# Kernel tuning notes

Hardware: AMD Instinct MI355X
Metric: run time of the kernel (lower is better)

The kernel has to match this reference:

```python
import jax, jax.numpy as jnp
import numpy as np


def setup_inputs() -> dict:
    key = jax.random.key(0)
    k1, k2 = jax.random.split(key)
    B, N, M = 4, 16384, 4096
    src_points = jax.random.normal(k1, (B, N, 3), dtype=jnp.float32)
    target_verts = jax.random.normal(k2, (B, M, 3), dtype=jnp.float32)
    return {"src_points": src_points, "target_verts": target_verts}


def reference(src_points, target_verts):
    # target_faces=None path of ChamferLoss: degenerate one-vertex triangles,
    # so closest-point-on-mesh == nearest target vertex.
    # d2[b,n,m] = ||p_bn - v_bm||^2 via the expansion p2 + v2 - 2 p.v
    p2 = jnp.sum(src_points * src_points, axis=-1)          # (B, N)
    v2 = jnp.sum(target_verts * target_verts, axis=-1)      # (B, M)
    pv = jnp.einsum('bnd,bmd->bnm', src_points, target_verts)  # (B, N, M)
    d2 = p2[:, :, None] + v2[:, None, :] - 2.0 * pv
    d2 = jnp.maximum(d2, 0.0)
    min_d2 = jnp.min(d2, axis=-1)                            # (B, N)
    num_src_per_batch = src_points.shape[1]
    loss = jnp.sum(min_d2, axis=-1) / num_src_per_batch      # (B,)
    return loss
```

## Files before the change

kernel.cpp:

```cpp
#include <hip/hip_runtime.h>
#include <float.h>


typedef __bf16 bf16x8 __attribute__((ext_vector_type(8)));
typedef float  f32x16 __attribute__((ext_vector_type(16)));

constexpr int B = 4, N = 16384, M = 4096;
constexpr int BN = B * N;
constexpr int TILES = M / 32;
constexpr int HT = TILES / 2;
constexpr int TPB = 512;
constexpr int PPB = 256;
constexpr int NPB = BN / PPB;

constexpr size_t VFRAG_BYTES = (size_t)B * M * 32;

__global__ __launch_bounds__(256) void chamfer_pre(
    const float* __restrict__ tv, unsigned char* __restrict__ vfr,
    float* __restrict__ out)
{
    if (blockIdx.x == 0 && threadIdx.x < B) out[threadIdx.x] = 0.0f;
    int i = blockIdx.x * 256 + threadIdx.x;
    float x = tv[3 * i + 0], y = tv[3 * i + 1], z = tv[3 * i + 2];
    __bf16 xh = (__bf16)x, yh = (__bf16)y, zh = (__bf16)z;
    float xhf = (float)xh, yhf = (float)yh, zhf = (float)zh;
    __bf16 xl = (__bf16)(x - xhf), yl = (__bf16)(y - yhf), zl = (__bf16)(z - zhf);
    float v2 = fmaf(x, x, fmaf(y, y, z * z));
    __bf16 v2h = (__bf16)v2;
    __bf16 v2l = (__bf16)(v2 - (float)v2h);
    __bf16 zero = (__bf16)0.0f;

    bf16x8 h0, h1;
    h0[0] = (__bf16)(-2.0f * xhf); h0[1] = (__bf16)(-2.0f * yhf);
    h0[2] = (__bf16)(-2.0f * zhf);
    h0[3] = h0[0]; h0[4] = h0[1]; h0[5] = h0[2];
    h0[6] = (__bf16)(-2.0f * (float)xl); h0[7] = (__bf16)(-2.0f * (float)yl);
    h1[0] = (__bf16)(-2.0f * (float)zl); h1[1] = v2h; h1[2] = v2l;
    h1[3] = zero; h1[4] = zero; h1[5] = zero; h1[6] = zero; h1[7] = zero;

    int m = i & (M - 1);
    size_t base = (size_t)(i >> 12) * 131072 + (size_t)(m >> 5) * 1024
                + (size_t)(m & 31) * 16;
    *(bf16x8*)(vfr + base)       = h0;
    *(bf16x8*)(vfr + base + 512) = h1;
}

__global__ __launch_bounds__(TPB) void chamfer_main(
    const float* __restrict__ src, const unsigned char* __restrict__ vfr,
    float* __restrict__ out)
{
    const int pblk = blockIdx.x;
    const int b    = pblk >> 6;
    const int t    = threadIdx.x;
    const int w    = t >> 6, L = t & 63;
    const int s    = w & 3, h = w >> 2;
    const int half = L >> 5, c = L & 31;
    const int laneoff = half * 512 + c * 16;

    const int P0 = pblk * PPB + s * 64;
    const int p0 = P0 + c, p1 = P0 + 32 + c;
    float x0 = src[3 * p0], y0 = src[3 * p0 + 1], z0 = src[3 * p0 + 2];
    float x1 = src[3 * p1], y1 = src[3 * p1 + 1], z1 = src[3 * p1 + 2];
    float pp0 = fmaf(x0, x0, fmaf(y0, y0, z0 * z0));
    float pp1 = fmaf(x1, x1, fmaf(y1, y1, z1 * z1));

    __bf16 one = (__bf16)1.0f, zero = (__bf16)0.0f;
    bf16x8 bP0, bP1;
    {
        __bf16 xh = (__bf16)x0, yh = (__bf16)y0, zh = (__bf16)z0;
        __bf16 xl = (__bf16)(x0 - (float)xh), yl = (__bf16)(y0 - (float)yh),
               zl = (__bf16)(z0 - (float)zh);
        if (half == 0) { bP0[0]=xh; bP0[1]=yh; bP0[2]=zh; bP0[3]=xl; bP0[4]=yl; bP0[5]=zl; bP0[6]=xh; bP0[7]=yh; }
        else { bP0[0]=zh; bP0[1]=one; bP0[2]=one; bP0[3]=zero; bP0[4]=zero; bP0[5]=zero; bP0[6]=zero; bP0[7]=zero; }
    }
    {
        __bf16 xh = (__bf16)x1, yh = (__bf16)y1, zh = (__bf16)z1;
        __bf16 xl = (__bf16)(x1 - (float)xh), yl = (__bf16)(y1 - (float)yh),
               zl = (__bf16)(z1 - (float)zh);
        if (half == 0) { bP1[0]=xh; bP1[1]=yh; bP1[2]=zh; bP1[3]=xl; bP1[4]=yl; bP1[5]=zl; bP1[6]=xh; bP1[7]=yh; }
        else { bP1[0]=zh; bP1[1]=one; bP1[2]=one; bP1[3]=zero; bP1[4]=zero; bP1[5]=zero; bP1[6]=zero; bP1[7]=zero; }
    }

    f32x16 zeroC;
#pragma unroll
    for (int r = 0; r < 16; ++r) zeroC[r] = 0.0f;
    float mn0[8], mn1[8];
#pragma unroll
    for (int u = 0; u < 8; ++u) { mn0[u] = FLT_MAX; mn1[u] = FLT_MAX; }

    const unsigned char* abase =
        vfr + (size_t)b * 131072 + (size_t)h * (HT * 1024) + laneoff;
#pragma unroll 8
    for (int tt = 0; tt < HT; ++tt) {
        bf16x8 av = *(const bf16x8*)(abase + tt * 1024);
        f32x16 C0 = __builtin_amdgcn_mfma_f32_32x32x16_bf16(av, bP0, zeroC, 0, 0, 0);
        f32x16 C1 = __builtin_amdgcn_mfma_f32_32x32x16_bf16(av, bP1, zeroC, 0, 0, 0);
#pragma unroll
        for (int u = 0; u < 8; ++u) {
            mn0[u] = fminf(fminf(mn0[u], C0[2 * u]), C0[2 * u + 1]);
            mn1[u] = fminf(fminf(mn1[u], C1[2 * u]), C1[2 * u + 1]);
        }
    }

    float a01 = fminf(fminf(mn0[0], mn0[1]), fminf(mn0[2], mn0[3]));
    float a23 = fminf(fminf(mn0[4], mn0[5]), fminf(mn0[6], mn0[7]));
    float m0 = fminf(a01, a23);
    m0 = fminf(m0, __shfl_xor(m0, 32, 64));
    float b01 = fminf(fminf(mn1[0], mn1[1]), fminf(mn1[2], mn1[3]));
    float b23 = fminf(fminf(mn1[4], mn1[5]), fminf(mn1[6], mn1[7]));
    float m1 = fminf(b01, b23);
    m1 = fminf(m1, __shfl_xor(m1, 32, 64));
    float m  = half ? m1 : m0;
    float pp = half ? pp1 : pp0;

    __shared__ float lds_m[TPB];
    __shared__ float acc[8];
    lds_m[t] = m;
    __syncthreads();

    float sum = 0.0f;
    if (w < 4) {
        float mm = fminf(m, lds_m[t + 256]);
        sum = fmaxf(mm + pp, 0.0f);
    }
    for (int off = 32; off > 0; off >>= 1)
        sum += __shfl_down(sum, off, 64);
    if (L == 0) acc[w] = sum;
    __syncthreads();
    if (t == 0) {
        float ssum = acc[0] + acc[1] + acc[2] + acc[3];
        atomicAdd(&out[b], ssum * (1.0f / N));
    }
}

extern "C" void kernel_launch(void* const* d_in, const int* in_sizes, int n_in,
                              void* d_out, int out_size, void* d_ws, size_t ws_size,
                              hipStream_t stream) {
    const float* src = (const float*)d_in[0];
    const float* tv  = (const float*)d_in[1];
    float* out = (float*)d_out;
    unsigned char* vfr = (unsigned char*)d_ws;

    chamfer_pre <<<(B * M) / 256, 256, 0, stream>>>(tv, vfr, out);
    chamfer_main<<<NPB, TPB, 0, stream>>>(src, vfr, out);
}
```

Measured before the change: 69.49 us.

## Fuse target-vertex preprocessing into main kernel via LDS chunks

```diff
diff --git a/kernel.cpp b/kernel.cpp
--- a/kernel.cpp
+++ b/kernel.cpp
@@ -7,48 +7,21 @@
 
 constexpr int B = 4, N = 16384, M = 4096;
 constexpr int BN = B * N;
-constexpr int TILES = M / 32;
-constexpr int HT = TILES / 2;
 constexpr int TPB = 512;
 constexpr int PPB = 256;
 constexpr int NPB = BN / PPB;
+constexpr int CHUNK = 2048;
+constexpr int NCH = M / CHUNK;
+constexpr int CT = CHUNK / 32;
+constexpr int HT = CT / 2;
 
-constexpr size_t VFRAG_BYTES = (size_t)B * M * 32;
-
-__global__ __launch_bounds__(256) void chamfer_pre(
-    const float* __restrict__ tv, unsigned char* __restrict__ vfr,
+__global__ __launch_bounds__(TPB) void chamfer_fused(
+    const float* __restrict__ src, const float* __restrict__ tv,
     float* __restrict__ out)
 {
-    if (blockIdx.x == 0 && threadIdx.x < B) out[threadIdx.x] = 0.0f;
-    int i = blockIdx.x * 256 + threadIdx.x;
-    float x = tv[3 * i + 0], y = tv[3 * i + 1], z = tv[3 * i + 2];
-    __bf16 xh = (__bf16)x, yh = (__bf16)y, zh = (__bf16)z;
-    float xhf = (float)xh, yhf = (float)yh, zhf = (float)zh;
-    __bf16 xl = (__bf16)(x - xhf), yl = (__bf16)(y - yhf), zl = (__bf16)(z - zhf);
-    float v2 = fmaf(x, x, fmaf(y, y, z * z));
-    __bf16 v2h = (__bf16)v2;
-    __bf16 v2l = (__bf16)(v2 - (float)v2h);
-    __bf16 zero = (__bf16)0.0f;
+    __shared__ uint4 lds4[4096];
+    char* ldsc = (char*)lds4;
 
-    bf16x8 h0, h1;
-    h0[0] = (__bf16)(-2.0f * xhf); h0[1] = (__bf16)(-2.0f * yhf);
-    h0[2] = (__bf16)(-2.0f * zhf);
-    h0[3] = h0[0]; h0[4] = h0[1]; h0[5] = h0[2];
-    h0[6] = (__bf16)(-2.0f * (float)xl); h0[7] = (__bf16)(-2.0f * (float)yl);
-    h1[0] = (__bf16)(-2.0f * (float)zl); h1[1] = v2h; h1[2] = v2l;
-    h1[3] = zero; h1[4] = zero; h1[5] = zero; h1[6] = zero; h1[7] = zero;
-
-    int m = i & (M - 1);
-    size_t base = (size_t)(i >> 12) * 131072 + (size_t)(m >> 5) * 1024
-                + (size_t)(m & 31) * 16;
-    *(bf16x8*)(vfr + base)       = h0;
-    *(bf16x8*)(vfr + base + 512) = h1;
-}
-
-__global__ __launch_bounds__(TPB) void chamfer_main(
-    const float* __restrict__ src, const unsigned char* __restrict__ vfr,
-    float* __restrict__ out)
-{
     const int pblk = blockIdx.x;
     const int b    = pblk >> 6;
     const int t    = threadIdx.x;
@@ -88,17 +61,47 @@
 #pragma unroll
     for (int u = 0; u < 8; ++u) { mn0[u] = FLT_MAX; mn1[u] = FLT_MAX; }
 
-    const unsigned char* abase =
-        vfr + (size_t)b * 131072 + (size_t)h * (HT * 1024) + laneoff;
+    for (int ch = 0; ch < NCH; ++ch) {
+        if (ch) __syncthreads();
+
+#pragma unroll
+        for (int k = 0; k < 4; ++k) {
+            int ml = t + k * 512;
+            int i  = b * M + ch * CHUNK + ml;
+            float x = tv[3 * i + 0], y = tv[3 * i + 1], z = tv[3 * i + 2];
+            __bf16 xh = (__bf16)x, yh = (__bf16)y, zh = (__bf16)z;
+            float xhf = (float)xh, yhf = (float)yh, zhf = (float)zh;
+            __bf16 xl = (__bf16)(x - xhf), yl = (__bf16)(y - yhf),
+                   zl = (__bf16)(z - zhf);
+            float v2 = fmaf(x, x, fmaf(y, y, z * z));
+            __bf16 v2h = (__bf16)v2;
+            __bf16 v2l = (__bf16)(v2 - (float)v2h);
+
+            bf16x8 h0, h1;
+            h0[0] = (__bf16)(-2.0f * xhf); h0[1] = (__bf16)(-2.0f * yhf);
+            h0[2] = (__bf16)(-2.0f * zhf);
+            h0[3] = h0[0]; h0[4] = h0[1]; h0[5] = h0[2];
+            h0[6] = (__bf16)(-2.0f * (float)xl); h0[7] = (__bf16)(-2.0f * (float)yl);
+            h1[0] = (__bf16)(-2.0f * (float)zl); h1[1] = v2h; h1[2] = v2l;
+            h1[3] = zero; h1[4] = zero; h1[5] = zero; h1[6] = zero; h1[7] = zero;
+
+            size_t base = (size_t)(ml >> 5) * 1024 + (size_t)(ml & 31) * 16;
+            *(bf16x8*)(ldsc + base)       = h0;
+            *(bf16x8*)(ldsc + base + 512) = h1;
+        }
+        __syncthreads();
+
+        const char* abase = ldsc + (size_t)h * (HT * 1024) + laneoff;
 #pragma unroll 8
-    for (int tt = 0; tt < HT; ++tt) {
-        bf16x8 av = *(const bf16x8*)(abase + tt * 1024);
-        f32x16 C0 = __builtin_amdgcn_mfma_f32_32x32x16_bf16(av, bP0, zeroC, 0, 0, 0);
-        f32x16 C1 = __builtin_amdgcn_mfma_f32_32x32x16_bf16(av, bP1, zeroC, 0, 0, 0);
+        for (int tt = 0; tt < HT; ++tt) {
+            bf16x8 av = *(const bf16x8*)(abase + tt * 1024);
+            f32x16 C0 = __builtin_amdgcn_mfma_f32_32x32x16_bf16(av, bP0, zeroC, 0, 0, 0);
+            f32x16 C1 = __builtin_amdgcn_mfma_f32_32x32x16_bf16(av, bP1, zeroC, 0, 0, 0);
 #pragma unroll
-        for (int u = 0; u < 8; ++u) {
-            mn0[u] = fminf(fminf(mn0[u], C0[2 * u]), C0[2 * u + 1]);
-            mn1[u] = fminf(fminf(mn1[u], C1[2 * u]), C1[2 * u + 1]);
+            for (int u = 0; u < 8; ++u) {
+                mn0[u] = fminf(fminf(mn0[u], C0[2 * u]), C0[2 * u + 1]);
+                mn1[u] = fminf(fminf(mn1[u], C1[2 * u]), C1[2 * u + 1]);
+            }
         }
     }
 
@@ -113,14 +116,15 @@
     float m  = half ? m1 : m0;
     float pp = half ? pp1 : pp0;
 
-    __shared__ float lds_m[TPB];
-    __shared__ float acc[8];
-    lds_m[t] = m;
+    __syncthreads();
+    float* lf = (float*)ldsc;
+    float* acc = lf + 512;
+    lf[t] = m;
     __syncthreads();
 
     float sum = 0.0f;
     if (w < 4) {
-        float mm = fminf(m, lds_m[t + 256]);
+        float mm = fminf(m, lf[t + 256]);
         sum = fmaxf(mm + pp, 0.0f);
     }
     for (int off = 32; off > 0; off >>= 1)
@@ -139,8 +143,7 @@
     const float* src = (const float*)d_in[0];
     const float* tv  = (const float*)d_in[1];
     float* out = (float*)d_out;
-    unsigned char* vfr = (unsigned char*)d_ws;
 
-    chamfer_pre <<<(B * M) / 256, 256, 0, stream>>>(tv, vfr, out);
-    chamfer_main<<<NPB, TPB, 0, stream>>>(src, vfr, out);
+    hipMemsetAsync(out, 0, out_size, stream);
+    chamfer_fused<<<NPB, TPB, 0, stream>>>(src, tv, out);
 }
```

Result: faster. 66.83 us (-3.8%).
